# Kernel tuning notes

Hardware: AMD Instinct MI355X
Metric: run time of the kernel (lower is better)

Reference implementation:

```python
import jax, jax.numpy as jnp
import numpy as np

N = 65536        # batch (nodes)
IN_SIZE = 256    # irreps1.dim * irreps2.dim = 16*16
OUT_SIZE = 256
NNZ = 2048       # nonzero Clebsch-Gordan entries


def setup_inputs() -> dict:
    key = jax.random.key(0)
    k1, k2, k3, k4 = jax.random.split(key, 4)
    inp = jax.random.normal(k1, (N, IN_SIZE), dtype=jnp.float32)
    scale = jax.random.normal(k2, (NNZ,), dtype=jnp.float32)
    M_in = jax.random.randint(k3, (NNZ,), 0, IN_SIZE, dtype=jnp.int64)
    M = jnp.sort(jax.random.randint(k4, (NNZ,), 0, OUT_SIZE, dtype=jnp.int64))
    return {"input": inp, "scale": scale, "M_in": M_in, "M": M, "out_size": OUT_SIZE}


def reference(input, scale, M_in, M, out_size):
    # sparse_scale: out[n, M[k]] += scale[k] * input[n, M_in[k]]
    gathered = input[:, M_in] * scale  # [N, nnz]
    # segment-sum over the nnz axis into out_size output slots (M is sorted)
    out = jax.ops.segment_sum(gathered.T, M, num_segments=out_size,
                              indices_are_sorted=True).T  # [N, out_size]
    return out
```

## Files before the change

kernel.cpp:

```cpp
#include <hip/hip_runtime.h>
#include <hip/hip_bf16.h>

#define IN_SZ   256
#define OUT_SZ  256
#define NNZ_C   2048
#define NB      16
#define BM      64
#define BK      64

typedef __attribute__((ext_vector_type(8))) short bf16x8;
typedef __attribute__((ext_vector_type(4))) float f32x4;

static __device__ __forceinline__ short f2bf(float f) {
    __hip_bfloat16 h = __float2bfloat16(f);
    return (short)__builtin_bit_cast(unsigned short, h);
}


__global__ void build_w(const float* __restrict__ scale,
                        const int*   __restrict__ M_in,
                        const int*   __restrict__ M,
                        unsigned short* __restrict__ wb)
{
    __shared__ float row[IN_SZ];
    const int j = blockIdx.x;
    const int t = threadIdx.x;

#pragma unroll
    for (int i = t; i < IN_SZ; i += 64) row[i] = 0.f;
    __syncthreads();

#pragma unroll
    for (int k = t; k < NNZ_C; k += 64)
        if (M[k] == j) atomicAdd(&row[M_in[k]], scale[k]);
    __syncthreads();

    const int wn = j >> 6, n = (j >> 4) & 3, l15 = j & 15;
#pragma unroll
    for (int kk = t; kk < IN_SZ; kk += 64) {
        int kt = kk >> 6, kf = (kk >> 5) & 1, lhi = (kk >> 3) & 3, e = kk & 7;
        int lane = lhi * 16 + l15;
        int c = (((wn * 4 + n) * 4 + kt) * 2 + kf) * 64 + lane;
        wb[c * 8 + e] = (unsigned short)f2bf(row[kk]);
    }
}


__global__ __launch_bounds__(256, 2)
void gemm_staged(const float* __restrict__ input,
                 const bf16x8* __restrict__ wfrag,
                 float* __restrict__ out)
{
    __shared__ float sA[2][BM * BK];

    const int tid  = threadIdx.x;
    const int lane = tid & 63;
    const int w    = tid >> 6;
    const int l15  = lane & 15, lhi = lane >> 4;
    const long row0 = (long)blockIdx.x * BM;

    f32x4 acc[4][4];
#pragma unroll
    for (int m = 0; m < 4; ++m)
#pragma unroll
        for (int n = 0; n < 4; ++n)
            acc[m][n] = (f32x4){0.f, 0.f, 0.f, 0.f};

    bf16x8 Breg[2][8];

    auto stage = [&](int buf, int kt) {
#pragma unroll
        for (int it = 0; it < 4; ++it) {
            const int c = w * 4 + it;
            const int r = c * 4 + lhi;
            const int s = l15 ^ (r & 7);
            const float* src = input + (row0 + r) * IN_SZ + kt * BK + s * 4;
            __builtin_amdgcn_global_load_lds(
                (const __attribute__((address_space(1))) unsigned int*)src,
                (__attribute__((address_space(3))) unsigned int*)&sA[buf][c * 256],
                16, 0, 0);
        }
    };

    stage(0, 0);
#pragma unroll
    for (int i = 0; i < 8; ++i)
        Breg[0][i] = wfrag[(((w * 4 + (i >> 1)) * 4 + 0) * 2 + (i & 1)) * 64 + lane];
    __syncthreads();

#pragma unroll
    for (int kt = 0; kt < 4; ++kt) {
        const int cur = kt & 1;
        if (kt < 3) {
#pragma unroll
            for (int i = 0; i < 8; ++i)
                Breg[cur ^ 1][i] =
                    wfrag[(((w * 4 + (i >> 1)) * 4 + (kt + 1)) * 2 + (i & 1)) * 64 + lane];
            stage(cur ^ 1, kt + 1);
        }

#pragma unroll
        for (int kf = 0; kf < 2; ++kf) {
#pragma unroll
            for (int m = 0; m < 4; ++m) {
                const int row = m * 16 + l15;
                const int s0  = kf * 8 + lhi * 2;
                const int i0  = row * BK + ((s0 ^ (row & 7)) << 2);
                const int i1  = row * BK + (((s0 + 1) ^ (row & 7)) << 2);
                f32x4 a0 = *(const f32x4*)&sA[cur][i0];
                f32x4 a1 = *(const f32x4*)&sA[cur][i1];
                bf16x8 u;
                u[0] = f2bf(a0[0]); u[1] = f2bf(a0[1]);
                u[2] = f2bf(a0[2]); u[3] = f2bf(a0[3]);
                u[4] = f2bf(a1[0]); u[5] = f2bf(a1[1]);
                u[6] = f2bf(a1[2]); u[7] = f2bf(a1[3]);
#pragma unroll
                for (int n = 0; n < 4; ++n)
                    acc[m][n] = __builtin_amdgcn_mfma_f32_16x16x32_bf16(
                        u, Breg[cur][n * 2 + kf], acc[m][n], 0, 0, 0);
            }
        }
        __syncthreads();
    }

#pragma unroll
    for (int m = 0; m < 4; ++m) {
        long r0 = row0 + m * 16 + lhi * 4;
#pragma unroll
        for (int n = 0; n < 4; ++n) {
            int col = w * 64 + n * 16 + l15;
#pragma unroll
            for (int r = 0; r < 4; ++r)
                out[(r0 + r) * OUT_SZ + col] = acc[m][n][r];
        }
    }
}


__global__ __launch_bounds__(256, 4)
void sparse_tp_kernel(const float* __restrict__ input,
                      const float* __restrict__ scale,
                      const int*   __restrict__ M_in,
                      const int*   __restrict__ M,
                      float*       __restrict__ out,
                      int N)
{
    __shared__ float s_in[NB * IN_SZ];
    __shared__ float s_scale[NNZ_C];
    __shared__ int   s_min[NNZ_C];
    __shared__ int   s_seg[OUT_SZ + 1];

    const int tid  = threadIdx.x;
    const int base = blockIdx.x * NB;

    {
        const float4* sc4  = reinterpret_cast<const float4*>(scale);
        const int4*   mi4  = reinterpret_cast<const int4*>(M_in);
        float4*       ssc4 = reinterpret_cast<float4*>(s_scale);
        int4*         smi4 = reinterpret_cast<int4*>(s_min);
        for (int v = tid; v < NNZ_C / 4; v += 256) { ssc4[v] = sc4[v]; smi4[v] = mi4[v]; }
    }
    {
        const float4* in4 = reinterpret_cast<const float4*>(input + (size_t)base * IN_SZ);
        float4*       si4 = reinterpret_cast<float4*>(s_in);
        for (int v = tid; v < NB * IN_SZ / 4; v += 256) {
            int row = v / (IN_SZ / 4);
            if (base + row < N) si4[v] = in4[v];
        }
    }
    {
        int j = tid, lo = 0, hi = NNZ_C;
        while (lo < hi) { int mid = (lo + hi) >> 1; if (M[mid] < j) lo = mid + 1; else hi = mid; }
        s_seg[j] = lo;
        if (tid == 0) s_seg[OUT_SZ] = NNZ_C;
    }
    __syncthreads();

    float acc[NB];
#pragma unroll
    for (int i = 0; i < NB; ++i) acc[i] = 0.f;

    const int j = tid;
    const int k1 = s_seg[j + 1];
    for (int k = s_seg[j]; k < k1; ++k) {
        const float s = s_scale[k];
        const int   m = s_min[k];
#pragma unroll
        for (int i = 0; i < NB; ++i) acc[i] += s * s_in[i * IN_SZ + m];
    }

    float* orow = out + (size_t)base * OUT_SZ + j;
#pragma unroll
    for (int i = 0; i < NB; ++i)
        if (base + i < N) orow[(size_t)i * OUT_SZ] = acc[i];
}


extern "C" void kernel_launch(void* const* d_in, const int* in_sizes, int n_in,
                              void* d_out, int out_size, void* d_ws, size_t ws_size,
                              hipStream_t stream)
{
    const float* input = (const float*)d_in[0];
    const float* scale = (const float*)d_in[1];
    const int*   M_in  = (const int*)d_in[2];
    const int*   M     = (const int*)d_in[3];
    float*       out   = (float*)d_out;

    const int N = in_sizes[0] / IN_SZ;

    if (ws_size >= (size_t)(128 * 1024) && (N % BM) == 0) {
        unsigned short* wb = (unsigned short*)d_ws;
        build_w    <<<OUT_SZ, 64, 0, stream>>>(scale, M_in, M, wb);
        gemm_staged<<<N / BM, 256, 0, stream>>>(input, (const bf16x8*)wb, out);
    } else {
        sparse_tp_kernel<<<(N + NB - 1) / NB, 256, 0, stream>>>(input, scale, M_in, M, out, N);
    }
}
```

Baseline: 139.8 us.

## Load full K tile into LDS once and binary-search segments in build_w

The GEMM kernel now copies the whole 64x256 fp32 input tile into LDS up front with one set of async global-to-LDS loads, replacing the double-buffered per-K-step staging. This removes the per-iteration barriers and the stage calls. The cost is 64 KB of LDS per block, which may limit how many blocks fit per CU, and there is no longer any overlap of load and compute across K steps. build_w now binary-searches the sorted M array for its segment and scans only those entries, instead of scanning all 2048 nonzeros per output column.

```diff
diff --git a/kernel.cpp b/kernel.cpp
--- a/kernel.cpp
+++ b/kernel.cpp
@@ -6,7 +6,7 @@
 #define NNZ_C   2048
 #define NB      16
 #define BM      64
-#define BK      64
+#define KFULL   256
 
 typedef __attribute__((ext_vector_type(8))) short bf16x8;
 typedef __attribute__((ext_vector_type(4))) float f32x4;
@@ -28,11 +28,15 @@
 
 #pragma unroll
     for (int i = t; i < IN_SZ; i += 64) row[i] = 0.f;
-    __syncthreads();
-
-#pragma unroll
-    for (int k = t; k < NNZ_C; k += 64)
-        if (M[k] == j) atomicAdd(&row[M_in[k]], scale[k]);
+
+    int lo = 0, hi = NNZ_C;
+    while (lo < hi) { int mid = (lo + hi) >> 1; if (M[mid] < j)     lo  = mid + 1; else hi  = mid; }
+    int lo2 = lo, hi2 = NNZ_C;
+    while (lo2 < hi2) { int mid = (lo2 + hi2) >> 1; if (M[mid] < j + 1) lo2 = mid + 1; else hi2 = mid; }
+
+    __syncthreads();
+    for (int k = lo + t; k < lo2; k += 64)
+        atomicAdd(&row[M_in[k]], scale[k]);
     __syncthreads();
 
     const int wn = j >> 6, n = (j >> 4) & 3, l15 = j & 15;
@@ -47,11 +51,11 @@
 
 
 __global__ __launch_bounds__(256, 2)
-void gemm_staged(const float* __restrict__ input,
-                 const bf16x8* __restrict__ wfrag,
-                 float* __restrict__ out)
-{
-    __shared__ float sA[2][BM * BK];
+void gemm_fullk(const float* __restrict__ input,
+                const bf16x8* __restrict__ wfrag,
+                float* __restrict__ out)
+{
+    __shared__ float sA[BM * KFULL];
 
     const int tid  = threadIdx.x;
     const int lane = tid & 63;
@@ -59,6 +63,16 @@
     const int l15  = lane & 15, lhi = lane >> 4;
     const long row0 = (long)blockIdx.x * BM;
 
+#pragma unroll
+    for (int it = 0; it < 16; ++it) {
+        const int r = w * 16 + it;
+        const float* src = input + (row0 + r) * IN_SZ + ((lane ^ (r & 7)) << 2);
+        __builtin_amdgcn_global_load_lds(
+            (const __attribute__((address_space(1))) unsigned int*)src,
+            (__attribute__((address_space(3))) unsigned int*)&sA[r * KFULL],
+            16, 0, 0);
+    }
+
     f32x4 acc[4][4];
 #pragma unroll
     for (int m = 0; m < 4; ++m)
@@ -67,25 +81,10 @@
             acc[m][n] = (f32x4){0.f, 0.f, 0.f, 0.f};
 
     bf16x8 Breg[2][8];
-
-    auto stage = [&](int buf, int kt) {
-#pragma unroll
-        for (int it = 0; it < 4; ++it) {
-            const int c = w * 4 + it;
-            const int r = c * 4 + lhi;
-            const int s = l15 ^ (r & 7);
-            const float* src = input + (row0 + r) * IN_SZ + kt * BK + s * 4;
-            __builtin_amdgcn_global_load_lds(
-                (const __attribute__((address_space(1))) unsigned int*)src,
-                (__attribute__((address_space(3))) unsigned int*)&sA[buf][c * 256],
-                16, 0, 0);
-        }
-    };
-
-    stage(0, 0);
 #pragma unroll
     for (int i = 0; i < 8; ++i)
         Breg[0][i] = wfrag[(((w * 4 + (i >> 1)) * 4 + 0) * 2 + (i & 1)) * 64 + lane];
+
     __syncthreads();
 
 #pragma unroll
@@ -96,19 +95,15 @@
             for (int i = 0; i < 8; ++i)
                 Breg[cur ^ 1][i] =
                     wfrag[(((w * 4 + (i >> 1)) * 4 + (kt + 1)) * 2 + (i & 1)) * 64 + lane];
-            stage(cur ^ 1, kt + 1);
-        }
-
+        }
 #pragma unroll
         for (int kf = 0; kf < 2; ++kf) {
 #pragma unroll
             for (int m = 0; m < 4; ++m) {
-                const int row = m * 16 + l15;
-                const int s0  = kf * 8 + lhi * 2;
-                const int i0  = row * BK + ((s0 ^ (row & 7)) << 2);
-                const int i1  = row * BK + (((s0 + 1) ^ (row & 7)) << 2);
-                f32x4 a0 = *(const f32x4*)&sA[cur][i0];
-                f32x4 a1 = *(const f32x4*)&sA[cur][i1];
+                const int r  = m * 16 + l15;
+                const int g0 = kt * 16 + kf * 8 + lhi * 2;
+                f32x4 a0 = *(const f32x4*)&sA[r * KFULL + ((g0 ^ (r & 7)) << 2)];
+                f32x4 a1 = *(const f32x4*)&sA[r * KFULL + (((g0 + 1) ^ (r & 7)) << 2)];
                 bf16x8 u;
                 u[0] = f2bf(a0[0]); u[1] = f2bf(a0[1]);
                 u[2] = f2bf(a0[2]); u[3] = f2bf(a0[3]);
@@ -120,7 +115,6 @@
                         u, Breg[cur][n * 2 + kf], acc[m][n], 0, 0, 0);
             }
         }
-        __syncthreads();
     }
 
 #pragma unroll
@@ -210,8 +204,8 @@
 
     if (ws_size >= (size_t)(128 * 1024) && (N % BM) == 0) {
         unsigned short* wb = (unsigned short*)d_ws;
-        build_w    <<<OUT_SZ, 64, 0, stream>>>(scale, M_in, M, wb);
-        gemm_staged<<<N / BM, 256, 0, stream>>>(input, (const bf16x8*)wb, out);
+        build_w   <<<OUT_SZ, 64, 0, stream>>>(scale, M_in, M, wb);
+        gemm_fullk<<<N / BM, 256, 0, stream>>>(input, (const bf16x8*)wb, out);
     } else {
         sparse_tp_kernel<<<(N + NB - 1) / NB, 256, 0, stream>>>(input, scale, M_in, M, out, N);
     }
```

Result: faster. 131.2 us (-6.2%).
